# Kernel optimization log

Hardware: AMD Instinct MI355X
Metric: run time of the kernel (lower is better)

The kernel has to match this reference:

```python
import jax, jax.numpy as jnp
import numpy as np
import math

IN_DIM = 256
OUT_DIM = 256
MAX_IN = 1024
MAX_OUT = 512
BATCH = 2
SEQ = 1024  # actual_seq_len == max_in_seq here
RED = 2
LN_EPS = 1e-5


def setup_inputs() -> dict:
    key = jax.random.key(0)
    ks = jax.random.split(key, 8)
    N = BATCH * SEQ
    return {
        "x": jax.random.normal(ks[0], (N, IN_DIM), dtype=jnp.float32),
        "M": jax.random.uniform(ks[1], (OUT_DIM, IN_DIM), minval=-0.5, maxval=0.5, dtype=jnp.float32),
        "P": jax.random.uniform(ks[2], (OUT_DIM, OUT_DIM), minval=-0.1, maxval=0.1, dtype=jnp.float32),
        "Linker": jax.random.uniform(ks[3], (MAX_IN, MAX_OUT), minval=-0.1, maxval=0.1, dtype=jnp.float32),
        "ln_gamma": jnp.ones((OUT_DIM,), dtype=jnp.float32),
        "ln_beta": jnp.zeros((OUT_DIM,), dtype=jnp.float32),
        "res_W": jax.random.uniform(ks[4], (OUT_DIM, IN_DIM), minval=-0.1, maxval=0.1, dtype=jnp.float32),
        "res_linker": jax.random.uniform(ks[5], (MAX_IN, MAX_OUT), minval=-0.1, maxval=0.1, dtype=jnp.float32),
        "actual_seq_len": SEQ,
    }


def _layer_norm(z, gamma, beta):
    mu = jnp.mean(z, axis=-1, keepdims=True)
    var = jnp.mean((z - mu) ** 2, axis=-1, keepdims=True)
    return (z - mu) * jax.lax.rsqrt(var + LN_EPS) * gamma + beta


def _periods():
    i = jnp.arange(OUT_DIM, dtype=jnp.float32)[:, None]
    j = jnp.arange(OUT_DIM, dtype=jnp.float32)[None, :]
    return i * OUT_DIM + j + 2.0  # (D, D)


def reference(x, M, P, Linker, ln_gamma, ln_beta, res_W, res_linker, actual_seq_len):
    S = int(actual_seq_len)
    N, _ = x.shape
    B = N // S
    D = OUT_DIM
    out_seq = max(1, S // RED)

    # Z = LN(x @ M^T)
    Z = _layer_norm(x @ M.T, ln_gamma, ln_beta)  # (N, D)

    # position transform: T[k,i] = sum_j Z[k,j] * P[i,j] * cos(2*pi*k / periods[i,j])
    k = jnp.arange(N, dtype=jnp.float32)[:, None, None]  # (N,1,1)
    phi = jnp.cos(2.0 * math.pi * k / _periods()[None])   # (N, D, D)
    T = jnp.einsum('kj,ij,kij->ki', Z, P, phi)            # (N, D)

    # adaptive sequence-length transform via Linker slice
    L = Linker[:S, :out_seq]                               # (S, out_seq)
    U = jnp.einsum('bsd,st->btd', T.reshape(B, S, D), L).reshape(B * out_seq, D)

    # 'separate' residual path
    rfeat = (x @ res_W.T).reshape(B, S, D)
    rL = res_linker[:S, :out_seq]
    residual = jnp.einsum('bsd,st->btd', rfeat, rL).reshape(B * out_seq, D)

    return U + residual
```

## Files before the change

kernel.cpp:

```cpp
#include <hip/hip_runtime.h>

#define D256 256
#define KT 8
#define S_SEQ 1024
#define OUTSEQ 512

__global__ __launch_bounds__(256) void k_prep(const float* __restrict__ M,
                                              const float* __restrict__ resW,
                                              const float* __restrict__ P,
                                              float2* __restrict__ MW,
                                              float4* __restrict__ PIt4) {
  const int j = blockIdx.x;
  const int t = threadIdx.x;
  MW[j * D256 + t] = make_float2(M[t * D256 + j], resW[t * D256 + j]);
  const float p = (float)(t * D256 + j + 2);
  const float ip = 1.0f / p;
  const float cb2 = 2.0f * __builtin_amdgcn_cosf(ip);
  PIt4[j * D256 + t] = make_float4(P[t * D256 + j], ip, cb2, 0.0f);
}

__global__ __launch_bounds__(1024, 4) void k_AB(const float* __restrict__ x,
                                                const float2* __restrict__ MW,
                                                const float4* __restrict__ PIt4,
                                                const float* __restrict__ gamma,
                                                const float* __restrict__ beta,
                                                float* __restrict__ T,
                                                float* __restrict__ rfeat) {
  __shared__ float Xs[D256][12];
  __shared__ float red[4][KT][D256];
  __shared__ float mu_s[KT], rs_s[KT];
  const int tid = threadIdx.x;
  const int i = tid & 255;
  const int h = tid >> 8;
  const int j0 = h * 64;
  const int k0 = blockIdx.x * KT;

  Xs[i][h]     = x[(k0 + h) * D256 + i];
  Xs[i][h + 4] = x[(k0 + h + 4) * D256 + i];
  __syncthreads();

  float aM[KT], aR[KT];
  #pragma unroll
  for (int r = 0; r < KT; ++r) { aM[r] = 0.f; aR[r] = 0.f; }
  {
    const float2* mwp = MW + i;
    #pragma unroll 8
    for (int jj = 0; jj < 64; ++jj) {
      const int j = j0 + jj;
      const float2 mw = mwp[j * D256];
      const float4 z0 = *(const float4*)&Xs[j][0];
      const float4 z1 = *(const float4*)&Xs[j][4];
      aM[0] = fmaf(z0.x, mw.x, aM[0]); aR[0] = fmaf(z0.x, mw.y, aR[0]);
      aM[1] = fmaf(z0.y, mw.x, aM[1]); aR[1] = fmaf(z0.y, mw.y, aR[1]);
      aM[2] = fmaf(z0.z, mw.x, aM[2]); aR[2] = fmaf(z0.z, mw.y, aR[2]);
      aM[3] = fmaf(z0.w, mw.x, aM[3]); aR[3] = fmaf(z0.w, mw.y, aR[3]);
      aM[4] = fmaf(z1.x, mw.x, aM[4]); aR[4] = fmaf(z1.x, mw.y, aR[4]);
      aM[5] = fmaf(z1.y, mw.x, aM[5]); aR[5] = fmaf(z1.y, mw.y, aR[5]);
      aM[6] = fmaf(z1.z, mw.x, aM[6]); aR[6] = fmaf(z1.z, mw.y, aR[6]);
      aM[7] = fmaf(z1.w, mw.x, aM[7]); aR[7] = fmaf(z1.w, mw.y, aR[7]);
    }
  }

  #pragma unroll
  for (int r = 0; r < KT; ++r) red[h][r][i] = aR[r];
  __syncthreads();
  #pragma unroll
  for (int p = 0; p < 2; ++p) {
    const int r = h * 2 + p;
    rfeat[(k0 + r) * D256 + i] =
        red[0][r][i] + red[1][r][i] + red[2][r][i] + red[3][r][i];
  }
  __syncthreads();

  #pragma unroll
  for (int r = 0; r < KT; ++r) red[h][r][i] = aM[r];
  __syncthreads();
  #pragma unroll
  for (int p = 0; p < 2; ++p) {
    const int r = h * 2 + p;
    Xs[i][r] = red[0][r][i] + red[1][r][i] + red[2][r][i] + red[3][r][i];
  }
  __syncthreads();

  const int w = tid >> 6, lane = tid & 63;
  if (w < KT) {
    float s = 0.f, sq = 0.f;
    #pragma unroll
    for (int l = 0; l < 4; ++l) {
      const float v = Xs[lane + 64 * l][w];
      s += v;
      sq = fmaf(v, v, sq);
    }
    #pragma unroll
    for (int off = 32; off; off >>= 1) {
      s += __shfl_down(s, off);
      sq += __shfl_down(sq, off);
    }
    if (lane == 0) {
      const float m = s * (1.0f / 256.0f);
      const float var = sq * (1.0f / 256.0f) - m * m;
      mu_s[w] = m;
      rs_s[w] = rsqrtf(var + 1e-5f);
    }
  }
  __syncthreads();
  {
    const float g = gamma[i], be = beta[i];
    #pragma unroll
    for (int p = 0; p < 2; ++p) {
      const int r = h + 4 * p;
      Xs[i][r] = (Xs[i][r] - mu_s[r]) * rs_s[r] * g + be;
    }
  }
  __syncthreads();

  float accT[KT] = {};
  const float kf0 = (float)k0, kf1 = (float)(k0 + 1);
  {
    const float4* pip = PIt4 + i;
    #pragma unroll 4
    for (int jj = 0; jj < 64; ++jj) {
      const int j = j0 + jj;
      const float4 pi = pip[j * D256];
      const float4 z0 = *(const float4*)&Xs[j][0];
      const float4 z1 = *(const float4*)&Xs[j][4];
      float r0 = kf0 * pi.y; r0 -= floorf(r0);
      float r1 = kf1 * pi.y; r1 -= floorf(r1);
      float c0 = __builtin_amdgcn_cosf(r0);
      float c1 = __builtin_amdgcn_cosf(r1);
      accT[0] = fmaf(z0.x * pi.x, c0, accT[0]);
      accT[1] = fmaf(z0.y * pi.x, c1, accT[1]);
      float c2;
      c2 = fmaf(pi.z, c1, -c0); accT[2] = fmaf(z0.z * pi.x, c2, accT[2]); c0 = c1; c1 = c2;
      c2 = fmaf(pi.z, c1, -c0); accT[3] = fmaf(z0.w * pi.x, c2, accT[3]); c0 = c1; c1 = c2;
      c2 = fmaf(pi.z, c1, -c0); accT[4] = fmaf(z1.x * pi.x, c2, accT[4]); c0 = c1; c1 = c2;
      c2 = fmaf(pi.z, c1, -c0); accT[5] = fmaf(z1.y * pi.x, c2, accT[5]); c0 = c1; c1 = c2;
      c2 = fmaf(pi.z, c1, -c0); accT[6] = fmaf(z1.z * pi.x, c2, accT[6]); c0 = c1; c1 = c2;
      c2 = fmaf(pi.z, c1, -c0); accT[7] = fmaf(z1.w * pi.x, c2, accT[7]);
    }
  }
  #pragma unroll
  for (int r = 0; r < KT; ++r) red[h][r][i] = accT[r];
  __syncthreads();
  #pragma unroll
  for (int p = 0; p < 2; ++p) {
    const int r = h * 2 + p;
    T[(k0 + r) * D256 + i] =
        red[0][r][i] + red[1][r][i] + red[2][r][i] + red[3][r][i];
  }
}

__global__ __launch_bounds__(256) void k_C1(const float* __restrict__ T,
                                            const float* __restrict__ rfeat,
                                            const float* __restrict__ Linker,
                                            const float* __restrict__ rLinker,
                                            float* __restrict__ part) {
  __shared__ float Ls[128][8];
  __shared__ float rLs[128][8];
  const int bid = blockIdx.x;
  const int sc = bid & 7;
  const int tt = (bid >> 3) & 63;
  const int b  = bid >> 9;
  const int t0 = tt * 8;
  const int s0 = sc * 128;
  const int d  = threadIdx.x;

  {
    const int row = threadIdx.x >> 1;
    const int c4  = (threadIdx.x & 1) * 4;
    *(float4*)&Ls[row][c4]  = *(const float4*)&Linker[(s0 + row) * OUTSEQ + t0 + c4];
    *(float4*)&rLs[row][c4] = *(const float4*)&rLinker[(s0 + row) * OUTSEQ + t0 + c4];
  }
  __syncthreads();

  float acc[8] = {};
  const float* Tp = &T[(b * S_SEQ + s0) * D256 + d];
  const float* Rp = &rfeat[(b * S_SEQ + s0) * D256 + d];
  #pragma unroll 4
  for (int s = 0; s < 128; ++s) {
    const float tv = Tp[s * D256];
    const float rv = Rp[s * D256];
    const float4 l0 = *(const float4*)&Ls[s][0];
    const float4 l1 = *(const float4*)&Ls[s][4];
    const float4 r0 = *(const float4*)&rLs[s][0];
    const float4 r1 = *(const float4*)&rLs[s][4];
    acc[0] = fmaf(tv, l0.x, acc[0]); acc[0] = fmaf(rv, r0.x, acc[0]);
    acc[1] = fmaf(tv, l0.y, acc[1]); acc[1] = fmaf(rv, r0.y, acc[1]);
    acc[2] = fmaf(tv, l0.z, acc[2]); acc[2] = fmaf(rv, r0.z, acc[2]);
    acc[3] = fmaf(tv, l0.w, acc[3]); acc[3] = fmaf(rv, r0.w, acc[3]);
    acc[4] = fmaf(tv, l1.x, acc[4]); acc[4] = fmaf(rv, r1.x, acc[4]);
    acc[5] = fmaf(tv, l1.y, acc[5]); acc[5] = fmaf(rv, r1.y, acc[5]);
    acc[6] = fmaf(tv, l1.z, acc[6]); acc[6] = fmaf(rv, r1.z, acc[6]);
    acc[7] = fmaf(tv, l1.w, acc[7]); acc[7] = fmaf(rv, r1.w, acc[7]);
  }

  const int rowbase = b * 512 + t0;
  #pragma unroll
  for (int u = 0; u < 8; ++u)
    part[(((sc << 10) + rowbase + u) << 8) + d] = acc[u];
}

__global__ __launch_bounds__(256) void k_C2(const float* __restrict__ part,
                                            float* __restrict__ out) {
  const int row = blockIdx.x;
  const int d   = threadIdx.x;
  float s = 0.f;
  #pragma unroll
  for (int sc = 0; sc < 8; ++sc)
    s += part[(((sc << 10) + row) << 8) + d];
  out[(row << 8) + d] = s;
}

extern "C" void kernel_launch(void* const* d_in, const int* in_sizes, int n_in,
                              void* d_out, int out_size, void* d_ws, size_t ws_size,
                              hipStream_t stream) {
  const float* x       = (const float*)d_in[0];
  const float* M       = (const float*)d_in[1];
  const float* P       = (const float*)d_in[2];
  const float* Linker  = (const float*)d_in[3];
  const float* gamma   = (const float*)d_in[4];
  const float* beta    = (const float*)d_in[5];
  const float* resW    = (const float*)d_in[6];
  const float* rLinker = (const float*)d_in[7];
  float* out = (float*)d_out;

  char* ws = (char*)d_ws;
  float2* MW    = (float2*)(ws);
  float4* PIt4  = (float4*)(ws + 512 * 1024);
  float*  T     = (float*)(ws + 1536 * 1024);
  float*  rfeat = (float*)(ws + 3584 * 1024);
  float*  part  = (float*)(ws + 5632 * 1024);

  hipLaunchKernelGGL(k_prep, dim3(256),  dim3(256),  0, stream, M, resW, P, MW, PIt4);
  hipLaunchKernelGGL(k_AB,   dim3(256),  dim3(1024), 0, stream, x, MW, PIt4, gamma, beta, T, rfeat);
  hipLaunchKernelGGL(k_C1,   dim3(1024), dim3(256),  0, stream, T, rfeat, Linker, rLinker, part);
  hipLaunchKernelGGL(k_C2,   dim3(1024), dim3(256),  0, stream, part, out);
}
```

Measured before the change: 61.59 us.

## Shrink period table to float2, merge reductions, widen C1 output tile

The precomputed P/period table goes from float4 to float2, and the Chebyshev recurrence coefficient is now recomputed in-loop with one extra cos. This halves the table's global traffic in k_AB. The two shared-memory reductions for rfeat and the M-projection are merged into one pass over float2 slots, removing a sync pair. k_C1 now computes 16 output columns per block instead of 8, with half the blocks, so T/rfeat are read half as often at the cost of more registers and fewer blocks.

```diff
diff --git a/kernel.cpp b/kernel.cpp
--- a/kernel.cpp
+++ b/kernel.cpp
@@ -9,25 +9,23 @@
                                               const float* __restrict__ resW,
                                               const float* __restrict__ P,
                                               float2* __restrict__ MW,
-                                              float4* __restrict__ PIt4) {
+                                              float2* __restrict__ PIt2) {
   const int j = blockIdx.x;
   const int t = threadIdx.x;
   MW[j * D256 + t] = make_float2(M[t * D256 + j], resW[t * D256 + j]);
   const float p = (float)(t * D256 + j + 2);
-  const float ip = 1.0f / p;
-  const float cb2 = 2.0f * __builtin_amdgcn_cosf(ip);
-  PIt4[j * D256 + t] = make_float4(P[t * D256 + j], ip, cb2, 0.0f);
+  PIt2[j * D256 + t] = make_float2(P[t * D256 + j], 1.0f / p);
 }
 
 __global__ __launch_bounds__(1024, 4) void k_AB(const float* __restrict__ x,
                                                 const float2* __restrict__ MW,
-                                                const float4* __restrict__ PIt4,
+                                                const float2* __restrict__ PIt2,
                                                 const float* __restrict__ gamma,
                                                 const float* __restrict__ beta,
                                                 float* __restrict__ T,
                                                 float* __restrict__ rfeat) {
   __shared__ float Xs[D256][12];
-  __shared__ float red[4][KT][D256];
+  __shared__ float2 red2[4][KT][D256];
   __shared__ float mu_s[KT], rs_s[KT];
   const int tid = threadIdx.x;
   const int i = tid & 255;
@@ -62,23 +60,15 @@
   }
 
   #pragma unroll
-  for (int r = 0; r < KT; ++r) red[h][r][i] = aR[r];
+  for (int r = 0; r < KT; ++r) red2[h][r][i] = make_float2(aM[r], aR[r]);
   __syncthreads();
   #pragma unroll
   for (int p = 0; p < 2; ++p) {
     const int r = h * 2 + p;
-    rfeat[(k0 + r) * D256 + i] =
-        red[0][r][i] + red[1][r][i] + red[2][r][i] + red[3][r][i];
-  }
-  __syncthreads();
-
-  #pragma unroll
-  for (int r = 0; r < KT; ++r) red[h][r][i] = aM[r];
-  __syncthreads();
-  #pragma unroll
-  for (int p = 0; p < 2; ++p) {
-    const int r = h * 2 + p;
-    Xs[i][r] = red[0][r][i] + red[1][r][i] + red[2][r][i] + red[3][r][i];
+    const float2 a0 = red2[0][r][i], a1 = red2[1][r][i];
+    const float2 a2 = red2[2][r][i], a3 = red2[3][r][i];
+    rfeat[(k0 + r) * D256 + i] = a0.y + a1.y + a2.y + a3.y;
+    Xs[i][r] = a0.x + a1.x + a2.x + a3.x;
   }
   __syncthreads();
 
@@ -117,36 +107,38 @@
   float accT[KT] = {};
   const float kf0 = (float)k0, kf1 = (float)(k0 + 1);
   {
-    const float4* pip = PIt4 + i;
-    #pragma unroll 4
+    const float2* pip = PIt2 + i;
+    #pragma unroll 8
     for (int jj = 0; jj < 64; ++jj) {
       const int j = j0 + jj;
-      const float4 pi = pip[j * D256];
+      const float2 pi = pip[j * D256];
       const float4 z0 = *(const float4*)&Xs[j][0];
       const float4 z1 = *(const float4*)&Xs[j][4];
-      float r0 = kf0 * pi.y; r0 -= floorf(r0);
-      float r1 = kf1 * pi.y; r1 -= floorf(r1);
+      const float cs = __builtin_amdgcn_cosf(pi.y);
+      const float cb2 = cs + cs;
+      const float r0 = __builtin_amdgcn_fractf(kf0 * pi.y);
+      const float r1 = __builtin_amdgcn_fractf(kf1 * pi.y);
       float c0 = __builtin_amdgcn_cosf(r0);
       float c1 = __builtin_amdgcn_cosf(r1);
       accT[0] = fmaf(z0.x * pi.x, c0, accT[0]);
       accT[1] = fmaf(z0.y * pi.x, c1, accT[1]);
       float c2;
-      c2 = fmaf(pi.z, c1, -c0); accT[2] = fmaf(z0.z * pi.x, c2, accT[2]); c0 = c1; c1 = c2;
-      c2 = fmaf(pi.z, c1, -c0); accT[3] = fmaf(z0.w * pi.x, c2, accT[3]); c0 = c1; c1 = c2;
-      c2 = fmaf(pi.z, c1, -c0); accT[4] = fmaf(z1.x * pi.x, c2, accT[4]); c0 = c1; c1 = c2;
-      c2 = fmaf(pi.z, c1, -c0); accT[5] = fmaf(z1.y * pi.x, c2, accT[5]); c0 = c1; c1 = c2;
-      c2 = fmaf(pi.z, c1, -c0); accT[6] = fmaf(z1.z * pi.x, c2, accT[6]); c0 = c1; c1 = c2;
-      c2 = fmaf(pi.z, c1, -c0); accT[7] = fmaf(z1.w * pi.x, c2, accT[7]);
-    }
-  }
-  #pragma unroll
-  for (int r = 0; r < KT; ++r) red[h][r][i] = accT[r];
+      c2 = fmaf(cb2, c1, -c0); accT[2] = fmaf(z0.z * pi.x, c2, accT[2]); c0 = c1; c1 = c2;
+      c2 = fmaf(cb2, c1, -c0); accT[3] = fmaf(z0.w * pi.x, c2, accT[3]); c0 = c1; c1 = c2;
+      c2 = fmaf(cb2, c1, -c0); accT[4] = fmaf(z1.x * pi.x, c2, accT[4]); c0 = c1; c1 = c2;
+      c2 = fmaf(cb2, c1, -c0); accT[5] = fmaf(z1.y * pi.x, c2, accT[5]); c0 = c1; c1 = c2;
+      c2 = fmaf(cb2, c1, -c0); accT[6] = fmaf(z1.z * pi.x, c2, accT[6]); c0 = c1; c1 = c2;
+      c2 = fmaf(cb2, c1, -c0); accT[7] = fmaf(z1.w * pi.x, c2, accT[7]);
+    }
+  }
+  #pragma unroll
+  for (int r = 0; r < KT; ++r) red2[h][r][i].x = accT[r];
   __syncthreads();
   #pragma unroll
   for (int p = 0; p < 2; ++p) {
     const int r = h * 2 + p;
     T[(k0 + r) * D256 + i] =
-        red[0][r][i] + red[1][r][i] + red[2][r][i] + red[3][r][i];
+        red2[0][r][i].x + red2[1][r][i].x + red2[2][r][i].x + red2[3][r][i].x;
   }
 }
 
@@ -155,48 +147,51 @@
                                             const float* __restrict__ Linker,
                                             const float* __restrict__ rLinker,
                                             float* __restrict__ part) {
-  __shared__ float Ls[128][8];
-  __shared__ float rLs[128][8];
+  __shared__ float Ls[128][16];
+  __shared__ float rLs[128][16];
   const int bid = blockIdx.x;
   const int sc = bid & 7;
-  const int tt = (bid >> 3) & 63;
-  const int b  = bid >> 9;
-  const int t0 = tt * 8;
+  const int tt = (bid >> 3) & 31;
+  const int b  = bid >> 8;
+  const int t0 = tt * 16;
   const int s0 = sc * 128;
   const int d  = threadIdx.x;
 
-  {
-    const int row = threadIdx.x >> 1;
-    const int c4  = (threadIdx.x & 1) * 4;
+  #pragma unroll
+  for (int it = 0; it < 2; ++it) {
+    const int idx = threadIdx.x + it * 256;
+    const int row = idx >> 2;
+    const int c4  = (idx & 3) * 4;
     *(float4*)&Ls[row][c4]  = *(const float4*)&Linker[(s0 + row) * OUTSEQ + t0 + c4];
     *(float4*)&rLs[row][c4] = *(const float4*)&rLinker[(s0 + row) * OUTSEQ + t0 + c4];
   }
   __syncthreads();
 
-  float acc[8] = {};
+  float acc[16] = {};
   const float* Tp = &T[(b * S_SEQ + s0) * D256 + d];
   const float* Rp = &rfeat[(b * S_SEQ + s0) * D256 + d];
   #pragma unroll 4
   for (int s = 0; s < 128; ++s) {
     const float tv = Tp[s * D256];
     const float rv = Rp[s * D256];
-    const float4 l0 = *(const float4*)&Ls[s][0];
-    const float4 l1 = *(const float4*)&Ls[s][4];
-    const float4 r0 = *(const float4*)&rLs[s][0];
-    const float4 r1 = *(const float4*)&rLs[s][4];
-    acc[0] = fmaf(tv, l0.x, acc[0]); acc[0] = fmaf(rv, r0.x, acc[0]);
-    acc[1] = fmaf(tv, l0.y, acc[1]); acc[1] = fmaf(rv, r0.y, acc[1]);
-    acc[2] = fmaf(tv, l0.z, acc[2]); acc[2] = fmaf(rv, r0.z, acc[2]);
-    acc[3] = fmaf(tv, l0.w, acc[3]); acc[3] = fmaf(rv, r0.w, acc[3]);
-    acc[4] = fmaf(tv, l1.x, acc[4]); acc[4] = fmaf(rv, r1.x, acc[4]);
-    acc[5] = fmaf(tv, l1.y, acc[5]); acc[5] = fmaf(rv, r1.y, acc[5]);
-    acc[6] = fmaf(tv, l1.z, acc[6]); acc[6] = fmaf(rv, r1.z, acc[6]);
-    acc[7] = fmaf(tv, l1.w, acc[7]); acc[7] = fmaf(rv, r1.w, acc[7]);
+    #pragma unroll
+    for (int q = 0; q < 4; ++q) {
+      const float4 l = *(const float4*)&Ls[s][q * 4];
+      const float4 r = *(const float4*)&rLs[s][q * 4];
+      acc[q * 4 + 0] = fmaf(tv, l.x, acc[q * 4 + 0]);
+      acc[q * 4 + 0] = fmaf(rv, r.x, acc[q * 4 + 0]);
+      acc[q * 4 + 1] = fmaf(tv, l.y, acc[q * 4 + 1]);
+      acc[q * 4 + 1] = fmaf(rv, r.y, acc[q * 4 + 1]);
+      acc[q * 4 + 2] = fmaf(tv, l.z, acc[q * 4 + 2]);
+      acc[q * 4 + 2] = fmaf(rv, r.z, acc[q * 4 + 2]);
+      acc[q * 4 + 3] = fmaf(tv, l.w, acc[q * 4 + 3]);
+      acc[q * 4 + 3] = fmaf(rv, r.w, acc[q * 4 + 3]);
+    }
   }
 
   const int rowbase = b * 512 + t0;
   #pragma unroll
-  for (int u = 0; u < 8; ++u)
+  for (int u = 0; u < 16; ++u)
     part[(((sc << 10) + rowbase + u) << 8) + d] = acc[u];
 }
 
@@ -226,13 +221,13 @@
 
   char* ws = (char*)d_ws;
   float2* MW    = (float2*)(ws);
-  float4* PIt4  = (float4*)(ws + 512 * 1024);
-  float*  T     = (float*)(ws + 1536 * 1024);
-  float*  rfeat = (float*)(ws + 3584 * 1024);
-  float*  part  = (float*)(ws + 5632 * 1024);
-
-  hipLaunchKernelGGL(k_prep, dim3(256),  dim3(256),  0, stream, M, resW, P, MW, PIt4);
-  hipLaunchKernelGGL(k_AB,   dim3(256),  dim3(1024), 0, stream, x, MW, PIt4, gamma, beta, T, rfeat);
-  hipLaunchKernelGGL(k_C1,   dim3(1024), dim3(256),  0, stream, T, rfeat, Linker, rLinker, part);
+  float2* PIt2  = (float2*)(ws + 512 * 1024);
+  float*  T     = (float*)(ws + 1024 * 1024);
+  float*  rfeat = (float*)(ws + 3072 * 1024);
+  float*  part  = (float*)(ws + 5120 * 1024);
+
+  hipLaunchKernelGGL(k_prep, dim3(256),  dim3(256),  0, stream, M, resW, P, MW, PIt2);
+  hipLaunchKernelGGL(k_AB,   dim3(256),  dim3(1024), 0, stream, x, MW, PIt2, gamma, beta, T, rfeat);
+  hipLaunchKernelGGL(k_C1,   dim3(512),  dim3(256),  0, stream, T, rfeat, Linker, rLinker, part);
   hipLaunchKernelGGL(k_C2,   dim3(1024), dim3(256),  0, stream, part, out);
 }
```

Result: slower. 62.99 us (+2.3%).
